# Performance work log

Measured on AMD Instinct MI355X. Metric: run time of the kernel, lower is better.

The kernel has to match this reference:

```python
import jax, jax.numpy as jnp
import numpy as np

D_MODEL = 1024
N_EXPERTS = 8
HIDDEN = 2048
TOP_K = 2


def setup_inputs() -> dict:
    key = jax.random.key(0)
    ks = jax.random.split(key, 5)
    scale_in = 1.0 / np.sqrt(D_MODEL)
    scale_h = 1.0 / np.sqrt(HIDDEN)
    return {
        "x": jax.random.normal(ks[0], (2, 2048, D_MODEL), dtype=jnp.float32),
        "w_router": jax.random.normal(ks[1], (D_MODEL, N_EXPERTS), dtype=jnp.float32) * scale_in,
        "w1": jax.random.normal(ks[2], (N_EXPERTS, D_MODEL, HIDDEN), dtype=jnp.float32) * scale_in,
        "w3": jax.random.normal(ks[3], (N_EXPERTS, D_MODEL, HIDDEN), dtype=jnp.float32) * scale_in,
        "w2": jax.random.normal(ks[4], (N_EXPERTS, HIDDEN, D_MODEL), dtype=jnp.float32) * scale_h,
    }


def reference(x, w_router, w1, w3, w2):
    orig_shape = x.shape
    xt = x.reshape(-1, orig_shape[-1])            # [T, D]
    T = xt.shape[0]

    # Router: linear -> softmax -> top-k (weights = top-k softmax scores)
    logits = xt @ w_router                         # [T, E]
    scores = jax.nn.softmax(logits, axis=-1)       # [T, E]
    top_w, top_idx = jax.lax.top_k(scores, TOP_K)  # [T, K]

    # Dense routing-weight matrix (reference form of dispatch/combine)
    dense_w = jnp.zeros((T, N_EXPERTS), dtype=scores.dtype)
    dense_w = dense_w.at[jnp.arange(T)[:, None], top_idx].set(top_w)  # [T, E]

    # Per-expert SwiGLU MLP over all tokens (dense reference of grouped GEMM)
    h1 = jnp.einsum('td,edh->teh', xt, w1)         # [T, E, H]
    h3 = jnp.einsum('td,edh->teh', xt, w3)
    h = jax.nn.silu(h1) * h3                       # [T, E, H]
    y = jnp.einsum('teh,ehd->ted', h, w2)          # [T, E, D]

    # Combine with routing weights
    out = jnp.einsum('te,ted->td', dense_w, y)     # [T, D]
    return out.reshape(orig_shape)
```

## Files before the change

### kernel.cpp

```cpp
#include <hip/hip_runtime.h>
#include <stdint.h>

#define D_MODEL 1024
#define N_EXP   8
#define HIDDEN  2048
#define TOPK    2

#define BK    64
#define PADM  128
#define NT1   (D_MODEL / BK)
#define NT2   (HIDDEN / BK)
#define G1X   1152
#define G2X   288

typedef short bf16x8 __attribute__((ext_vector_type(8)));
typedef float f32x4 __attribute__((ext_vector_type(4)));

__device__ __forceinline__ unsigned short f2bf(float f) {
    union { float f; unsigned u; } v; v.f = f;
    unsigned r = v.u + 0x7fffu + ((v.u >> 16) & 1u);
    return (unsigned short)(r >> 16);
}

__device__ __forceinline__ float bf2f(unsigned short u) {
    union { unsigned u; float f; } v; v.u = (unsigned)u << 16; return v.f;
}

__device__ __forceinline__ void gload_lds16(const void* g, void* l) {
    __builtin_amdgcn_global_load_lds(
        (const __attribute__((address_space(1))) void*)g,
        (__attribute__((address_space(3))) void*)l, 16, 0, 0);
}

__global__ __launch_bounds__(256) void k_prep(
    const float* __restrict__ x, const float* __restrict__ wr,
    const float* __restrict__ w1, const float* __restrict__ w3, const float* __restrict__ w2,
    unsigned short* __restrict__ xb,
    unsigned short* __restrict__ w13t, unsigned short* __restrict__ w2t,
    int* __restrict__ tok_e, float* __restrict__ tok_w,
    int* __restrict__ counts, int T, int nrouter)
{
    __shared__ unsigned short tls[64][68];
    const int bx = blockIdx.x;
    const int tid = threadIdx.x;

    if (bx < nrouter) {
        int t = bx * 4 + (tid >> 6);
        int lane = tid & 63;
        if (t >= T) return;
        const float4* xr = (const float4*)(x + (size_t)t * D_MODEL);
        float acc[N_EXP];
#pragma unroll
        for (int e = 0; e < N_EXP; ++e) acc[e] = 0.f;
#pragma unroll
        for (int j = 0; j < 4; ++j) {
            int c = j * 64 + lane;
            float4 v = xr[c];
            ushort4 pk;
            pk.x = f2bf(v.x); pk.y = f2bf(v.y); pk.z = f2bf(v.z); pk.w = f2bf(v.w);
            *(ushort4*)(xb + (size_t)t * D_MODEL + c * 4) = pk;
            const float4* w4 = (const float4*)(wr + (size_t)c * 4 * N_EXP);
#pragma unroll
            for (int k = 0; k < 4; ++k) {
                float xv = (k == 0) ? v.x : (k == 1) ? v.y : (k == 2) ? v.z : v.w;
                float4 wa = w4[k * 2], wb = w4[k * 2 + 1];
                acc[0] += xv * wa.x; acc[1] += xv * wa.y; acc[2] += xv * wa.z; acc[3] += xv * wa.w;
                acc[4] += xv * wb.x; acc[5] += xv * wb.y; acc[6] += xv * wb.z; acc[7] += xv * wb.w;
            }
        }
#pragma unroll
        for (int off = 32; off > 0; off >>= 1) {
#pragma unroll
            for (int e = 0; e < N_EXP; ++e) acc[e] += __shfl_down(acc[e], off, 64);
        }
        if (lane == 0) {
            float mx = acc[0];
#pragma unroll
            for (int e = 1; e < N_EXP; ++e) mx = fmaxf(mx, acc[e]);
            float p[N_EXP], den = 0.f;
#pragma unroll
            for (int e = 0; e < N_EXP; ++e) { p[e] = __expf(acc[e] - mx); den += p[e]; }
            float inv = 1.f / den;
            int e0 = 0; float v0 = acc[0];
#pragma unroll
            for (int e = 1; e < N_EXP; ++e) if (acc[e] > v0) { v0 = acc[e]; e0 = e; }
            int e1 = -1; float v1 = -1e30f;
#pragma unroll
            for (int e = 0; e < N_EXP; ++e) if (e != e0 && acc[e] > v1) { v1 = acc[e]; e1 = e; }
            tok_e[2 * t] = e0;     tok_w[2 * t] = p[e0] * inv;
            tok_e[2 * t + 1] = e1; tok_w[2 * t + 1] = p[e1] * inv;
            atomicAdd(&counts[e0], 1);
            atomicAdd(&counts[e1], 1);
        }
        return;
    }

    const int b2 = bx - nrouter;
    const int z = b2 >> 9;
    const int inner = b2 & 511;
    const int mat = z >> 3, e = z & 7;
    const float* in; int Rr, Cc;
    if (mat == 0)      { in = w1; Rr = D_MODEL; Cc = HIDDEN; }
    else if (mat == 1) { in = w3; Rr = D_MODEL; Cc = HIDDEN; }
    else               { in = w2; Rr = HIDDEN; Cc = D_MODEL; }
    const size_t eb_in = (size_t)e * Rr * Cc;
    const int tpc = Cc >> 6;
    const int c0 = (inner % tpc) * 64, r0 = (inner / tpc) * 64;
#pragma unroll
    for (int p = 0; p < 4; ++p) {
        int li = p * 256 + tid;
        int r = li >> 4, q = li & 15;
        float4 v = *(const float4*)(in + eb_in + (size_t)(r0 + r) * Cc + c0 + q * 4);
        tls[q * 4 + 0][r] = f2bf(v.x);
        tls[q * 4 + 1][r] = f2bf(v.y);
        tls[q * 4 + 2][r] = f2bf(v.z);
        tls[q * 4 + 3][r] = f2bf(v.w);
    }
    __syncthreads();
    if (mat < 2) {
        const size_t eb = (size_t)e * (2 * HIDDEN) * D_MODEL;
        const int moff = mat ? 16 : 0;
#pragma unroll
        for (int p = 0; p < 2; ++p) {
            int li = p * 256 + tid;
            int c = li >> 3, j = li & 7;
            int C = c0 + c;
            int r13 = ((C >> 4) << 5) + moff + (C & 15);
            bf16x8 v = *(const bf16x8*)(&tls[c][j * 8]);
            *(bf16x8*)(&w13t[eb + (size_t)r13 * D_MODEL + r0 + j * 8]) = v;
        }
    } else {
        const size_t eb = (size_t)e * D_MODEL * HIDDEN;
#pragma unroll
        for (int p = 0; p < 2; ++p) {
            int li = p * 256 + tid;
            int c = li >> 3, j = li & 7;
            bf16x8 v = *(const bf16x8*)(&tls[c][j * 8]);
            *(bf16x8*)(&w2t[eb + (size_t)(c0 + c) * HIDDEN + r0 + j * 8]) = v;
        }
    }
}

__global__ void k_scan_scatter(const int* __restrict__ counts,
                               const int* __restrict__ tok_e, const float* __restrict__ tok_w,
                               int* __restrict__ offs,
                               int* __restrict__ row_token, float* __restrict__ row_weight,
                               int* __restrict__ tok_pos, int T) {
    __shared__ int scurs[N_EXP];
    if (threadIdx.x == 0) {
        int s = 0;
        for (int e = 0; e < N_EXP; ++e) {
            offs[e] = s; scurs[e] = s;
            s += ((counts[e] + PADM - 1) / PADM) * PADM;
        }
        offs[N_EXP] = s;
    }
    __syncthreads();
    for (int i = threadIdx.x; i < 2 * T; i += blockDim.x) {
        int e = tok_e[i];
        int pos = atomicAdd(&scurs[e], 1);
        row_token[pos] = i >> 1;
        row_weight[pos] = tok_w[i];
        tok_pos[i] = pos;
    }
}

__global__ __launch_bounds__(512, 1) void k_gemm1(
    const unsigned short* __restrict__ xb,
    const unsigned short* __restrict__ w13t,
    const int* __restrict__ row_token,
    const float* __restrict__ row_weight,
    const int* __restrict__ offs,
    unsigned short* __restrict__ h)
{
    __shared__ unsigned short A[3][128 * BK];
    __shared__ unsigned short B[3][256 * BK];

    const int b = blockIdx.x;
    const int bs = (b & 7) * (G1X / 8) + (b >> 3);
    int e = 0, mt = 0, nt = 0, found = 0, at = 0;
#pragma unroll
    for (int ee = 0; ee < N_EXP; ++ee) {
        int me = (offs[ee + 1] - offs[ee]) >> 7;
        int te = me * 16;
        if (!found && bs < at + te) {
            int loc = bs - at;
            nt = loc / me;
            mt = loc - nt * me;
            e = ee; found = 1;
        }
        at += te;
    }
    if (!found) return;
    const int m0 = offs[e] + mt * 128;
    const int n0b = nt * 256;

    const int tid = threadIdx.x;
    const int lane = tid & 63, wid = tid >> 6;
    const int wm = wid >> 2, wn = wid & 3;

    const unsigned short* asrc[2];
    unsigned aoff[2];
#pragma unroll
    for (int q = 0; q < 2; ++q) {
        int c = q * 512 + tid;
        int m = c >> 3, kc = c & 7;
        int kcs = kc ^ (m & 7);
        int tok = row_token[m0 + m];
        asrc[q] = xb + (size_t)tok * D_MODEL + kcs * 8;
        aoff[q] = (unsigned)c * 8u;
    }
    const unsigned short* bsrc[4];
    unsigned boff[4];
#pragma unroll
    for (int q = 0; q < 4; ++q) {
        int c = q * 512 + tid;
        int n = c >> 3, kc = c & 7;
        int kcs = kc ^ (n & 7);
        bsrc[q] = w13t + ((size_t)e * (2 * HIDDEN) + n0b + n) * D_MODEL + kcs * 8;
        boff[q] = (unsigned)c * 8u;
    }

    f32x4 acc[4][4];
    const f32x4 zf = {0.f, 0.f, 0.f, 0.f};
#pragma unroll
    for (int mi = 0; mi < 4; ++mi)
#pragma unroll
        for (int ni = 0; ni < 4; ++ni) acc[mi][ni] = zf;

#pragma unroll
    for (int t = 0; t < 2; ++t) {
        const int ko = t * BK;
        gload_lds16(asrc[0] + ko, &A[t][aoff[0]]);
        gload_lds16(asrc[1] + ko, &A[t][aoff[1]]);
        gload_lds16(bsrc[0] + ko, &B[t][boff[0]]);
        gload_lds16(bsrc[1] + ko, &B[t][boff[1]]);
        gload_lds16(bsrc[2] + ko, &B[t][boff[2]]);
        gload_lds16(bsrc[3] + ko, &B[t][boff[3]]);
    }

    int cur = 0;
#pragma unroll 1
    for (int kt = 0; kt < NT1; ++kt) {
        if (kt == NT1 - 1) asm volatile("s_waitcnt vmcnt(0)" ::: "memory");
        else               asm volatile("s_waitcnt vmcnt(6)" ::: "memory");
        __builtin_amdgcn_s_barrier();

        unsigned short* Ac = &A[cur][0];
        unsigned short* Bc = &B[cur][0];
        const int nb = (cur + 2 >= 3) ? (cur - 1) : (cur + 2);
        const int ko = (kt + 2) * BK;
        const bool pf = (kt + 2 < NT1);

        {
            bf16x8 a0[4], b0[4];
            int ke = (lane >> 4) * 8;
#pragma unroll
            for (int mi = 0; mi < 4; ++mi) {
                int m = wm * 64 + mi * 16 + (lane & 15);
                a0[mi] = *(const bf16x8*)(&Ac[m * BK + (ke ^ ((m & 7) * 8))]);
            }
#pragma unroll
            for (int ni = 0; ni < 4; ++ni) {
                int n = wn * 64 + ni * 16 + (lane & 15);
                b0[ni] = *(const bf16x8*)(&Bc[n * BK + (ke ^ ((n & 7) * 8))]);
            }
            if (pf) {
                gload_lds16(asrc[0] + ko, &A[nb][aoff[0]]);
                gload_lds16(asrc[1] + ko, &A[nb][aoff[1]]);
                gload_lds16(bsrc[0] + ko, &B[nb][boff[0]]);
            }
            __builtin_amdgcn_s_barrier();
            __builtin_amdgcn_s_setprio(1);
#pragma unroll
            for (int mi = 0; mi < 4; ++mi)
#pragma unroll
                for (int ni = 0; ni < 4; ++ni)
                    acc[mi][ni] = __builtin_amdgcn_mfma_f32_16x16x32_bf16(a0[mi], b0[ni], acc[mi][ni], 0, 0, 0);
            __builtin_amdgcn_s_setprio(0);
        }
        {
            bf16x8 a1[4], b1[4];
            int ke = 32 + (lane >> 4) * 8;
#pragma unroll
            for (int mi = 0; mi < 4; ++mi) {
                int m = wm * 64 + mi * 16 + (lane & 15);
                a1[mi] = *(const bf16x8*)(&Ac[m * BK + (ke ^ ((m & 7) * 8))]);
            }
#pragma unroll
            for (int ni = 0; ni < 4; ++ni) {
                int n = wn * 64 + ni * 16 + (lane & 15);
                b1[ni] = *(const bf16x8*)(&Bc[n * BK + (ke ^ ((n & 7) * 8))]);
            }
            if (pf) {
                gload_lds16(bsrc[1] + ko, &B[nb][boff[1]]);
                gload_lds16(bsrc[2] + ko, &B[nb][boff[2]]);
                gload_lds16(bsrc[3] + ko, &B[nb][boff[3]]);
            }
            __builtin_amdgcn_s_barrier();
            __builtin_amdgcn_s_setprio(1);
#pragma unroll
            for (int mi = 0; mi < 4; ++mi)
#pragma unroll
                for (int ni = 0; ni < 4; ++ni)
                    acc[mi][ni] = __builtin_amdgcn_mfma_f32_16x16x32_bf16(a1[mi], b1[ni], acc[mi][ni], 0, 0, 0);
            __builtin_amdgcn_s_setprio(0);
        }
        cur = (cur == 2) ? 0 : (cur + 1);
    }

    const int g0 = (n0b + wn * 64) >> 5;
#pragma unroll
    for (int mi = 0; mi < 4; ++mi) {
#pragma unroll
        for (int r = 0; r < 4; ++r) {
            int m = wm * 64 + mi * 16 + (lane >> 4) * 4 + r;
            float wgt = row_weight[m0 + m];
            size_t rowbase = (size_t)(m0 + m) * HIDDEN;
#pragma unroll
            for (int p = 0; p < 2; ++p) {
                float v1 = acc[mi][2 * p][r], v3 = acc[mi][2 * p + 1][r];
                float sv = v1 / (1.f + __expf(-v1));
                int hc = (g0 + p) * 16 + (lane & 15);
                h[rowbase + hc] = f2bf(sv * v3 * wgt);
            }
        }
    }
}

__global__ __launch_bounds__(512, 1) void k_gemm2(
    const unsigned short* __restrict__ h,
    const unsigned short* __restrict__ w2t,
    const int* __restrict__ offs,
    unsigned short* __restrict__ y)
{
    __shared__ unsigned short A[3][128 * BK];
    __shared__ unsigned short B[3][256 * BK];

    const int b = blockIdx.x;
    const int bs = (b & 7) * (G2X / 8) + (b >> 3);
    int e = 0, mt = 0, nt = 0, found = 0, at = 0;
#pragma unroll
    for (int ee = 0; ee < N_EXP; ++ee) {
        int me = (offs[ee + 1] - offs[ee]) >> 7;
        int te = me * 4;
        if (!found && bs < at + te) {
            int loc = bs - at;
            nt = loc / me;
            mt = loc - nt * me;
            e = ee; found = 1;
        }
        at += te;
    }
    if (!found) return;
    const int m0 = offs[e] + mt * 128;
    const int n0 = nt * 256;

    const int tid = threadIdx.x;
    const int lane = tid & 63, wid = tid >> 6;
    const int wm = wid >> 2, wn = wid & 3;

    const unsigned short* asrc[2];
    unsigned aoff[2];
#pragma unroll
    for (int q = 0; q < 2; ++q) {
        int c = q * 512 + tid;
        int m = c >> 3, kc = c & 7;
        int kcs = kc ^ (m & 7);
        asrc[q] = h + (size_t)(m0 + m) * HIDDEN + kcs * 8;
        aoff[q] = (unsigned)c * 8u;
    }
    const unsigned short* bsrc[4];
    unsigned boff[4];
#pragma unroll
    for (int q = 0; q < 4; ++q) {
        int c = q * 512 + tid;
        int n = c >> 3, kc = c & 7;
        int kcs = kc ^ (n & 7);
        bsrc[q] = w2t + ((size_t)e * D_MODEL + n0 + n) * HIDDEN + kcs * 8;
        boff[q] = (unsigned)c * 8u;
    }

    f32x4 acc[4][4];
    const f32x4 zf = {0.f, 0.f, 0.f, 0.f};
#pragma unroll
    for (int mi = 0; mi < 4; ++mi)
#pragma unroll
        for (int ni = 0; ni < 4; ++ni) acc[mi][ni] = zf;

#pragma unroll
    for (int t = 0; t < 2; ++t) {
        const int ko = t * BK;
        gload_lds16(asrc[0] + ko, &A[t][aoff[0]]);
        gload_lds16(asrc[1] + ko, &A[t][aoff[1]]);
        gload_lds16(bsrc[0] + ko, &B[t][boff[0]]);
        gload_lds16(bsrc[1] + ko, &B[t][boff[1]]);
        gload_lds16(bsrc[2] + ko, &B[t][boff[2]]);
        gload_lds16(bsrc[3] + ko, &B[t][boff[3]]);
    }

    int cur = 0;
#pragma unroll 1
    for (int kt = 0; kt < NT2; ++kt) {
        if (kt == NT2 - 1) asm volatile("s_waitcnt vmcnt(0)" ::: "memory");
        else               asm volatile("s_waitcnt vmcnt(6)" ::: "memory");
        __builtin_amdgcn_s_barrier();

        unsigned short* Ac = &A[cur][0];
        unsigned short* Bc = &B[cur][0];
        const int nb = (cur + 2 >= 3) ? (cur - 1) : (cur + 2);
        const int ko = (kt + 2) * BK;
        const bool pf = (kt + 2 < NT2);

        {
            bf16x8 a0[4], b0[4];
            int ke = (lane >> 4) * 8;
#pragma unroll
            for (int mi = 0; mi < 4; ++mi) {
                int m = wm * 64 + mi * 16 + (lane & 15);
                a0[mi] = *(const bf16x8*)(&Ac[m * BK + (ke ^ ((m & 7) * 8))]);
            }
#pragma unroll
            for (int ni = 0; ni < 4; ++ni) {
                int n = wn * 64 + ni * 16 + (lane & 15);
                b0[ni] = *(const bf16x8*)(&Bc[n * BK + (ke ^ ((n & 7) * 8))]);
            }
            if (pf) {
                gload_lds16(asrc[0] + ko, &A[nb][aoff[0]]);
                gload_lds16(asrc[1] + ko, &A[nb][aoff[1]]);
                gload_lds16(bsrc[0] + ko, &B[nb][boff[0]]);
            }
            __builtin_amdgcn_s_barrier();
            __builtin_amdgcn_s_setprio(1);
#pragma unroll
            for (int mi = 0; mi < 4; ++mi)
#pragma unroll
                for (int ni = 0; ni < 4; ++ni)
                    acc[mi][ni] = __builtin_amdgcn_mfma_f32_16x16x32_bf16(a0[mi], b0[ni], acc[mi][ni], 0, 0, 0);
            __builtin_amdgcn_s_setprio(0);
        }
        {
            bf16x8 a1[4], b1[4];
            int ke = 32 + (lane >> 4) * 8;
#pragma unroll
            for (int mi = 0; mi < 4; ++mi) {
                int m = wm * 64 + mi * 16 + (lane & 15);
                a1[mi] = *(const bf16x8*)(&Ac[m * BK + (ke ^ ((m & 7) * 8))]);
            }
#pragma unroll
            for (int ni = 0; ni < 4; ++ni) {
                int n = wn * 64 + ni * 16 + (lane & 15);
                b1[ni] = *(const bf16x8*)(&Bc[n * BK + (ke ^ ((n & 7) * 8))]);
            }
            if (pf) {
                gload_lds16(bsrc[1] + ko, &B[nb][boff[1]]);
                gload_lds16(bsrc[2] + ko, &B[nb][boff[2]]);
                gload_lds16(bsrc[3] + ko, &B[nb][boff[3]]);
            }
            __builtin_amdgcn_s_barrier();
            __builtin_amdgcn_s_setprio(1);
#pragma unroll
            for (int mi = 0; mi < 4; ++mi)
#pragma unroll
                for (int ni = 0; ni < 4; ++ni)
                    acc[mi][ni] = __builtin_amdgcn_mfma_f32_16x16x32_bf16(a1[mi], b1[ni], acc[mi][ni], 0, 0, 0);
            __builtin_amdgcn_s_setprio(0);
        }
        cur = (cur == 2) ? 0 : (cur + 1);
    }

#pragma unroll
    for (int mi = 0; mi < 4; ++mi) {
#pragma unroll
        for (int r = 0; r < 4; ++r) {
            int m = wm * 64 + mi * 16 + (lane >> 4) * 4 + r;
            size_t rowbase = (size_t)(m0 + m) * D_MODEL + n0;
#pragma unroll
            for (int ni = 0; ni < 4; ++ni) {
                int n = wn * 64 + ni * 16 + (lane & 15);
                y[rowbase + n] = f2bf(acc[mi][ni][r]);
            }
        }
    }
}

__global__ void k_combine(const unsigned short* __restrict__ y,
                          const int* __restrict__ tok_pos,
                          float* __restrict__ out, int n8) {
    int i = blockIdx.x * blockDim.x + threadIdx.x;
    if (i >= n8) return;
    int t = i >> 7;
    int c = (i & 127) * 8;
    int p0 = tok_pos[2 * t];
    int p1 = tok_pos[2 * t + 1];
    bf16x8 v0 = *(const bf16x8*)(y + (size_t)p0 * D_MODEL + c);
    bf16x8 v1 = *(const bf16x8*)(y + (size_t)p1 * D_MODEL + c);
    float* op = out + (size_t)t * D_MODEL + c;
    float4 o0, o1;
    o0.x = bf2f((unsigned short)v0[0]) + bf2f((unsigned short)v1[0]);
    o0.y = bf2f((unsigned short)v0[1]) + bf2f((unsigned short)v1[1]);
    o0.z = bf2f((unsigned short)v0[2]) + bf2f((unsigned short)v1[2]);
    o0.w = bf2f((unsigned short)v0[3]) + bf2f((unsigned short)v1[3]);
    o1.x = bf2f((unsigned short)v0[4]) + bf2f((unsigned short)v1[4]);
    o1.y = bf2f((unsigned short)v0[5]) + bf2f((unsigned short)v1[5]);
    o1.z = bf2f((unsigned short)v0[6]) + bf2f((unsigned short)v1[6]);
    o1.w = bf2f((unsigned short)v0[7]) + bf2f((unsigned short)v1[7]);
    *(float4*)op = o0;
    *(float4*)(op + 4) = o1;
}

extern "C" void kernel_launch(void* const* d_in, const int* in_sizes, int n_in,
                              void* d_out, int out_size, void* d_ws, size_t ws_size,
                              hipStream_t stream) {
    const float* x  = (const float*)d_in[0];
    const float* wr = (const float*)d_in[1];
    const float* w1 = (const float*)d_in[2];
    const float* w3 = (const float*)d_in[3];
    const float* w2 = (const float*)d_in[4];
    float* out = (float*)d_out;

    const int T = in_sizes[0] / D_MODEL;
    const int Rp = T * TOPK + N_EXP * PADM;

    char* ws = (char*)d_ws;
    size_t o = 0;
    unsigned short* xb   = (unsigned short*)(ws + o); o += (size_t)T * D_MODEL * 2;
    unsigned short* h    = (unsigned short*)(ws + o); o += (size_t)Rp * HIDDEN * 2;
    unsigned short* w13t = (unsigned short*)(ws + o); o += (size_t)N_EXP * 2 * HIDDEN * D_MODEL * 2;
    unsigned short* w2t  = (unsigned short*)(ws + o); o += (size_t)N_EXP * D_MODEL * HIDDEN * 2;
    int*   row_token  = (int*)(ws + o);   o += (size_t)Rp * 4;
    float* row_weight = (float*)(ws + o); o += (size_t)Rp * 4;
    int*   tok_e      = (int*)(ws + o);   o += (size_t)2 * T * 4;
    float* tok_w      = (float*)(ws + o); o += (size_t)2 * T * 4;
    int*   tok_pos    = (int*)(ws + o);   o += (size_t)2 * T * 4;
    int*   counts     = (int*)(ws + o);   o += 16 * 4;
    int*   offs       = (int*)(ws + o);   o += 16 * 4;

    unsigned short* y = w13t;

    hipMemsetAsync(counts, 0, 16 * 4, stream);
    hipMemsetAsync(row_token, 0, (size_t)Rp * 4, stream);
    hipMemsetAsync(row_weight, 0, (size_t)Rp * 4, stream);

    const int nrouter = (T + 3) / 4;
    const int nprep = nrouter + 24 * 512;
    k_prep<<<nprep, 256, 0, stream>>>(x, wr, w1, w3, w2, xb, w13t, w2t,
                                      tok_e, tok_w, counts, T, nrouter);

    k_scan_scatter<<<1, 1024, 0, stream>>>(counts, tok_e, tok_w, offs,
                                           row_token, row_weight, tok_pos, T);

    k_gemm1<<<G1X, 512, 0, stream>>>(xb, w13t, row_token, row_weight, offs, h);
    k_gemm2<<<G2X, 512, 0, stream>>>(h, w2t, offs, y);

    int n8 = T * D_MODEL / 8;
    k_combine<<<(n8 + 255) / 256, 256, 0, stream>>>(y, tok_pos, out, n8);
}
```

Measured before the change: 329.2 us.

## Split prep kernel and rewrite weight transpose with wide tiles and packed bf16 conversion

Splits the fused router/weight-prep kernel into a router kernel and a dedicated weight transpose kernel. The transpose now uses 512 blocks that each stream a 64-row slab over many column strips, with 16 float4 loads per thread held in flight. It converts pairs with the hardware v_cvt_pk_bf16_f32 instruction, stages in an XOR-swizzled LDS tile, and writes 16-byte vectors. The aim is higher bandwidth and fewer conversion instructions for the large fp32-to-bf16 weight transposition. It adds a kernel launch, and the low block count may limit occupancy.

```diff
diff --git a/kernel.cpp b/kernel.cpp
--- a/kernel.cpp
+++ b/kernel.cpp
@@ -15,6 +15,7 @@
 
 typedef short bf16x8 __attribute__((ext_vector_type(8)));
 typedef float f32x4 __attribute__((ext_vector_type(4)));
+typedef unsigned u32x4 __attribute__((ext_vector_type(4)));
 
 __device__ __forceinline__ unsigned short f2bf(float f) {
     union { float f; unsigned u; } v; v.f = f;
@@ -26,117 +27,134 @@
     union { unsigned u; float f; } v; v.u = (unsigned)u << 16; return v.f;
 }
 
+__device__ __forceinline__ unsigned cvtpk(float a, float b) {
+    unsigned r;
+    asm("v_cvt_pk_bf16_f32 %0, %1, %2" : "=v"(r) : "v"(a), "v"(b));
+    return r;
+}
+
 __device__ __forceinline__ void gload_lds16(const void* g, void* l) {
     __builtin_amdgcn_global_load_lds(
         (const __attribute__((address_space(1))) void*)g,
         (__attribute__((address_space(3))) void*)l, 16, 0, 0);
 }
 
-__global__ __launch_bounds__(256) void k_prep(
+__global__ __launch_bounds__(256) void k_pre(
     const float* __restrict__ x, const float* __restrict__ wr,
+    unsigned short* __restrict__ xb,
+    int* __restrict__ tok_e, float* __restrict__ tok_w,
+    int* __restrict__ counts, int T)
+{
+    int t = blockIdx.x * 4 + (threadIdx.x >> 6);
+    int lane = threadIdx.x & 63;
+    if (t >= T) return;
+    const float4* xr = (const float4*)(x + (size_t)t * D_MODEL);
+    float acc[N_EXP];
+#pragma unroll
+    for (int e = 0; e < N_EXP; ++e) acc[e] = 0.f;
+#pragma unroll
+    for (int j = 0; j < 4; ++j) {
+        int c = j * 64 + lane;
+        float4 v = xr[c];
+        ushort4 pk;
+        pk.x = f2bf(v.x); pk.y = f2bf(v.y); pk.z = f2bf(v.z); pk.w = f2bf(v.w);
+        *(ushort4*)(xb + (size_t)t * D_MODEL + c * 4) = pk;
+        const float4* w4 = (const float4*)(wr + (size_t)c * 4 * N_EXP);
+#pragma unroll
+        for (int k = 0; k < 4; ++k) {
+            float xv = (k == 0) ? v.x : (k == 1) ? v.y : (k == 2) ? v.z : v.w;
+            float4 wa = w4[k * 2], wb = w4[k * 2 + 1];
+            acc[0] += xv * wa.x; acc[1] += xv * wa.y; acc[2] += xv * wa.z; acc[3] += xv * wa.w;
+            acc[4] += xv * wb.x; acc[5] += xv * wb.y; acc[6] += xv * wb.z; acc[7] += xv * wb.w;
+        }
+    }
+#pragma unroll
+    for (int off = 32; off > 0; off >>= 1) {
+#pragma unroll
+        for (int e = 0; e < N_EXP; ++e) acc[e] += __shfl_down(acc[e], off, 64);
+    }
+    if (lane == 0) {
+        float mx = acc[0];
+#pragma unroll
+        for (int e = 1; e < N_EXP; ++e) mx = fmaxf(mx, acc[e]);
+        float p[N_EXP], den = 0.f;
+#pragma unroll
+        for (int e = 0; e < N_EXP; ++e) { p[e] = __expf(acc[e] - mx); den += p[e]; }
+        float inv = 1.f / den;
+        int e0 = 0; float v0 = acc[0];
+#pragma unroll
+        for (int e = 1; e < N_EXP; ++e) if (acc[e] > v0) { v0 = acc[e]; e0 = e; }
+        int e1 = -1; float v1 = -1e30f;
+#pragma unroll
+        for (int e = 0; e < N_EXP; ++e) if (e != e0 && acc[e] > v1) { v1 = acc[e]; e1 = e; }
+        tok_e[2 * t] = e0;     tok_w[2 * t] = p[e0] * inv;
+        tok_e[2 * t + 1] = e1; tok_w[2 * t + 1] = p[e1] * inv;
+        atomicAdd(&counts[e0], 1);
+        atomicAdd(&counts[e1], 1);
+    }
+}
+
+__global__ __launch_bounds__(256) void k_wt(
     const float* __restrict__ w1, const float* __restrict__ w3, const float* __restrict__ w2,
-    unsigned short* __restrict__ xb,
-    unsigned short* __restrict__ w13t, unsigned short* __restrict__ w2t,
-    int* __restrict__ tok_e, float* __restrict__ tok_w,
-    int* __restrict__ counts, int T, int nrouter)
+    unsigned short* __restrict__ w13t, unsigned short* __restrict__ w2t)
 {
-    __shared__ unsigned short tls[64][68];
+    __shared__ unsigned tile[256][32];
     const int bx = blockIdx.x;
     const int tid = threadIdx.x;
-
-    if (bx < nrouter) {
-        int t = bx * 4 + (tid >> 6);
-        int lane = tid & 63;
-        if (t >= T) return;
-        const float4* xr = (const float4*)(x + (size_t)t * D_MODEL);
-        float acc[N_EXP];
-#pragma unroll
-        for (int e = 0; e < N_EXP; ++e) acc[e] = 0.f;
+    const int w = tid >> 6, lane = tid & 63;
+
+    const float* in; int Cc, nstr, r0, e, moff; bool is13;
+    if (bx < 256) {
+        int z = bx >> 4;
+        int mat = z >> 3; e = z & 7;
+        in = (mat ? w3 : w1) + (size_t)e * D_MODEL * HIDDEN;
+        Cc = HIDDEN; nstr = 8;
+        r0 = (bx & 15) * 64;
+        is13 = true; moff = mat ? 16 : 0;
+    } else {
+        int b2 = bx - 256;
+        e = b2 >> 5;
+        in = w2 + (size_t)e * HIDDEN * D_MODEL;
+        Cc = D_MODEL; nstr = 4;
+        r0 = (b2 & 31) * 64;
+        is13 = false; moff = 0;
+    }
+
+    for (int s = 0; s < nstr; ++s) {
+        const int cs = s * 256;
+        f32x4 v[16];
+#pragma unroll
+        for (int i = 0; i < 16; ++i) {
+            int r = w * 16 + i;
+            v[i] = *(const f32x4*)(in + (size_t)(r0 + r) * Cc + cs + lane * 4);
+        }
+        if (s) __syncthreads();
 #pragma unroll
         for (int j = 0; j < 4; ++j) {
-            int c = j * 64 + lane;
-            float4 v = xr[c];
-            ushort4 pk;
-            pk.x = f2bf(v.x); pk.y = f2bf(v.y); pk.z = f2bf(v.z); pk.w = f2bf(v.w);
-            *(ushort4*)(xb + (size_t)t * D_MODEL + c * 4) = pk;
-            const float4* w4 = (const float4*)(wr + (size_t)c * 4 * N_EXP);
-#pragma unroll
-            for (int k = 0; k < 4; ++k) {
-                float xv = (k == 0) ? v.x : (k == 1) ? v.y : (k == 2) ? v.z : v.w;
-                float4 wa = w4[k * 2], wb = w4[k * 2 + 1];
-                acc[0] += xv * wa.x; acc[1] += xv * wa.y; acc[2] += xv * wa.z; acc[3] += xv * wa.w;
-                acc[4] += xv * wb.x; acc[5] += xv * wb.y; acc[6] += xv * wb.z; acc[7] += xv * wb.w;
-            }
-        }
-#pragma unroll
-        for (int off = 32; off > 0; off >>= 1) {
-#pragma unroll
-            for (int e = 0; e < N_EXP; ++e) acc[e] += __shfl_down(acc[e], off, 64);
-        }
-        if (lane == 0) {
-            float mx = acc[0];
-#pragma unroll
-            for (int e = 1; e < N_EXP; ++e) mx = fmaxf(mx, acc[e]);
-            float p[N_EXP], den = 0.f;
-#pragma unroll
-            for (int e = 0; e < N_EXP; ++e) { p[e] = __expf(acc[e] - mx); den += p[e]; }
-            float inv = 1.f / den;
-            int e0 = 0; float v0 = acc[0];
-#pragma unroll
-            for (int e = 1; e < N_EXP; ++e) if (acc[e] > v0) { v0 = acc[e]; e0 = e; }
-            int e1 = -1; float v1 = -1e30f;
-#pragma unroll
-            for (int e = 0; e < N_EXP; ++e) if (e != e0 && acc[e] > v1) { v1 = acc[e]; e1 = e; }
-            tok_e[2 * t] = e0;     tok_w[2 * t] = p[e0] * inv;
-            tok_e[2 * t + 1] = e1; tok_w[2 * t + 1] = p[e1] * inv;
-            atomicAdd(&counts[e0], 1);
-            atomicAdd(&counts[e1], 1);
-        }
-        return;
-    }
-
-    const int b2 = bx - nrouter;
-    const int z = b2 >> 9;
-    const int inner = b2 & 511;
-    const int mat = z >> 3, e = z & 7;
-    const float* in; int Rr, Cc;
-    if (mat == 0)      { in = w1; Rr = D_MODEL; Cc = HIDDEN; }
-    else if (mat == 1) { in = w3; Rr = D_MODEL; Cc = HIDDEN; }
-    else               { in = w2; Rr = HIDDEN; Cc = D_MODEL; }
-    const size_t eb_in = (size_t)e * Rr * Cc;
-    const int tpc = Cc >> 6;
-    const int c0 = (inner % tpc) * 64, r0 = (inner / tpc) * 64;
-#pragma unroll
-    for (int p = 0; p < 4; ++p) {
-        int li = p * 256 + tid;
-        int r = li >> 4, q = li & 15;
-        float4 v = *(const float4*)(in + eb_in + (size_t)(r0 + r) * Cc + c0 + q * 4);
-        tls[q * 4 + 0][r] = f2bf(v.x);
-        tls[q * 4 + 1][r] = f2bf(v.y);
-        tls[q * 4 + 2][r] = f2bf(v.z);
-        tls[q * 4 + 3][r] = f2bf(v.w);
-    }
-    __syncthreads();
-    if (mat < 2) {
-        const size_t eb = (size_t)e * (2 * HIDDEN) * D_MODEL;
-        const int moff = mat ? 16 : 0;
-#pragma unroll
-        for (int p = 0; p < 2; ++p) {
-            int li = p * 256 + tid;
-            int c = li >> 3, j = li & 7;
-            int C = c0 + c;
-            int r13 = ((C >> 4) << 5) + moff + (C & 15);
-            bf16x8 v = *(const bf16x8*)(&tls[c][j * 8]);
-            *(bf16x8*)(&w13t[eb + (size_t)r13 * D_MODEL + r0 + j * 8]) = v;
-        }
-    } else {
-        const size_t eb = (size_t)e * D_MODEL * HIDDEN;
-#pragma unroll
-        for (int p = 0; p < 2; ++p) {
-            int li = p * 256 + tid;
-            int c = li >> 3, j = li & 7;
-            bf16x8 v = *(const bf16x8*)(&tls[c][j * 8]);
-            *(bf16x8*)(&w2t[eb + (size_t)(c0 + c) * HIDDEN + r0 + j * 8]) = v;
+            int c = lane * 4 + j;
+            unsigned sw = (((unsigned)c >> 2) & 7u) << 2;
+#pragma unroll
+            for (int p = 0; p < 8; ++p) {
+                tile[c][(unsigned)(w * 8 + p) ^ sw] = cvtpk(v[2 * p][j], v[2 * p + 1][j]);
+            }
+        }
+        __syncthreads();
+        {
+            int c = tid;
+            int C = cs + c;
+            unsigned sw = (((unsigned)c >> 2) & 7u) << 2;
+            unsigned short* outp;
+            if (is13) {
+                int r13 = ((C >> 4) << 5) + moff + (C & 15);
+                outp = w13t + ((size_t)e * (2 * HIDDEN) + r13) * D_MODEL + r0;
+            } else {
+                outp = w2t + ((size_t)e * D_MODEL + C) * HIDDEN + r0;
+            }
+#pragma unroll
+            for (int k = 0; k < 8; ++k) {
+                u32x4 d = *(const u32x4*)(&tile[c][(unsigned)(k * 4) ^ sw]);
+                *(u32x4*)(outp + k * 8) = d;
+            }
         }
     }
 }
@@ -542,10 +560,8 @@
     hipMemsetAsync(row_token, 0, (size_t)Rp * 4, stream);
     hipMemsetAsync(row_weight, 0, (size_t)Rp * 4, stream);
 
-    const int nrouter = (T + 3) / 4;
-    const int nprep = nrouter + 24 * 512;
-    k_prep<<<nprep, 256, 0, stream>>>(x, wr, w1, w3, w2, xb, w13t, w2t,
-                                      tok_e, tok_w, counts, T, nrouter);
+    k_pre<<<(T + 3) / 4, 256, 0, stream>>>(x, wr, xb, tok_e, tok_w, counts, T);
+    k_wt<<<512, 256, 0, stream>>>(w1, w3, w2, w13t, w2t);
 
     k_scan_scatter<<<1, 1024, 0, stream>>>(counts, tok_e, tok_w, offs,
                                            row_token, row_weight, tok_pos, T);
```

Result: slower. 367.5 us (+11.7%).
